# Kernel optimization log

Measured on AMD Instinct MI355X. Metric: run time of the kernel, lower is better.

## Reference

```python
import jax, jax.numpy as jnp
import numpy as np

B, N, NE = 16, 96, 256
ATOM, EDIM, HID, LAT, HEADS = 128, 16, 128, 128, 4
HD = LAT // HEADS
RBF, CUT, ZEMB, MAXZ = 16, 5.0, 32, 100
MUL0_IN, MUL1_IN = 64, 32      # irreps_node = 64x0e + 32x1o (dim 160)
MUL0_OUT, MUL1_OUT = 32, 16    # out irreps  = 32x0e + 16x1o (dim 80)
NODE_DIM = MUL0_IN + 3 * MUL1_IN
OUT_DIM = MUL0_OUT + 3 * MUL1_OUT
E_ATT = 1024
WNUM = MUL0_IN*MUL0_OUT + MUL0_IN*MUL1_OUT + MUL1_IN*MUL1_OUT + MUL1_IN*MUL0_OUT  # 4608


def _mlp3(x, w1, b1, w2, b2, w3, b3):
    x = jax.nn.silu(x @ w1 + b1)
    x = jax.nn.silu(x @ w2 + b2)
    return x @ w3 + b3


def setup_inputs() -> dict:
    key = jax.random.key(0)
    ks = jax.random.split(key, 40)
    s = 0.05  # scale params so deep MLP activations stay numerically sane
    d = {}
    d['h'] = jax.random.normal(ks[0], (B, N, ATOM), jnp.float32)
    d['h_full'] = jax.random.normal(ks[1], (B, N, NODE_DIM), jnp.float32)
    d['e_feat'] = jax.random.normal(ks[2], (NE, EDIM), jnp.float32)
    d['att_dist'] = jax.random.uniform(ks[3], (E_ATT,), jnp.float32)
    d['att_vec'] = jax.random.normal(ks[4], (E_ATT, 3), jnp.float32)
    d['z_emb_table'] = jax.random.normal(ks[5], (MAXZ + 1, ZEMB), jnp.float32) * s
    d['rw1'] = jax.random.normal(ks[6], (ZEMB + 1 + RBF, HID), jnp.float32) * s
    d['rb1'] = jnp.zeros((HID,), jnp.float32)
    d['rw2'] = jax.random.normal(ks[7], (HID, WNUM), jnp.float32) * s
    d['rb2'] = jnp.zeros((WNUM,), jnp.float32)
    d['ew1'] = jax.random.normal(ks[8], (EDIM, HID), jnp.float32) * s
    d['eb1'] = jnp.zeros((HID,), jnp.float32)
    d['ew2'] = jax.random.normal(ks[9], (HID, MUL0_OUT + MUL1_OUT), jnp.float32) * s
    d['eb2'] = jnp.zeros((MUL0_OUT + MUL1_OUT,), jnp.float32)
    d['qw1'] = jax.random.normal(ks[10], (ATOM + EDIM, HID), jnp.float32) * s
    d['qb1'] = jnp.zeros((HID,), jnp.float32)
    d['qw2'] = jax.random.normal(ks[11], (HID, HID), jnp.float32) * s
    d['qb2'] = jnp.zeros((HID,), jnp.float32)
    d['qw3'] = jax.random.normal(ks[12], (HID, LAT), jnp.float32) * s
    d['qb3'] = jnp.zeros((LAT,), jnp.float32)
    d['kw1'] = jax.random.normal(ks[13], (ATOM + ZEMB + 1 + RBF, HID), jnp.float32) * s
    d['kb1'] = jnp.zeros((HID,), jnp.float32)
    d['kw2'] = jax.random.normal(ks[14], (HID, HID), jnp.float32) * s
    d['kb2'] = jnp.zeros((HID,), jnp.float32)
    d['kw3'] = jax.random.normal(ks[15], (HID, LAT), jnp.float32) * s
    d['kb3'] = jnp.zeros((LAT,), jnp.float32)
    d['ow1'] = jax.random.normal(ks[16], (MUL0_OUT + MUL1_OUT, HID), jnp.float32) * s
    d['ob1'] = jnp.zeros((HID,), jnp.float32)
    d['ow2'] = jax.random.normal(ks[17], (HID, HID), jnp.float32) * s
    d['ob2'] = jnp.zeros((HID,), jnp.float32)
    d['ow3'] = jax.random.normal(ks[18], (HID, LAT), jnp.float32) * s
    d['ob3'] = jnp.zeros((LAT,), jnp.float32)
    d['z'] = jax.random.randint(ks[19], (B, N), 0, MAXZ)
    d['mask'] = jnp.ones((B, N), bool)
    d['absorber_index'] = jax.random.randint(ks[20], (B,), 0, N)
    d['att_dst'] = jnp.arange(E_ATT)  # unique flat indices into B*N
    return d


def reference(h, h_full, e_feat, att_dist, att_vec, z_emb_table,
              rw1, rb1, rw2, rb2, ew1, eb1, ew2, eb2,
              qw1, qb1, qw2, qb2, qw3, qb3,
              kw1, kb1, kw2, kb2, kw3, kb3,
              ow1, ob1, ow2, ob2, ow3, ob3,
              z, mask, absorber_index, att_dst):
    Bz, Na, Hd = h.shape
    F = Bz * Na
    nE = e_feat.shape[0]
    # scatter edge data into flat (B*N) atom slots
    am_flat = jnp.zeros((F,), bool).at[att_dst].set(True)
    d_flat = jnp.zeros((F,), h.dtype).at[att_dst].set(att_dist)
    v_flat = jnp.zeros((F, 3), h.dtype).at[att_dst].set(att_vec)
    att_mask = am_flat.reshape(Bz, Na) & mask
    # spherical harmonics (lmax=1, component normalization): Y0 = 1, Y1 = sqrt(3)*unit_vec
    un = v_flat / jnp.maximum(jnp.linalg.norm(v_flat, axis=-1, keepdims=True), 1e-8)
    y1 = jnp.sqrt(3.0) * un
    # Gaussian RBF on absorber->atom distance
    mu = jnp.linspace(0.0, CUT, RBF)
    delta = CUT / (RBF - 1)
    rbf = jnp.exp(-(d_flat[:, None] - mu) ** 2 / (2.0 * delta * delta))  # (F, RBF)
    zr = z_emb_table[z]                      # (B, N, ZEMB)
    zr_flat = zr.reshape(F, -1)
    is_abs = jnp.zeros((Bz, Na), h.dtype).at[jnp.arange(Bz), absorber_index].set(1.0)
    # radial MLP -> per-edge tensor-product weights
    w_in = jnp.concatenate([zr_flat, is_abs.reshape(F, 1), rbf], -1)
    tpw = jax.nn.silu(w_in @ rw1 + rb1) @ rw2 + rb2  # (F, WNUM)
    s1 = MUL0_IN * MUL0_OUT
    s2 = s1 + MUL0_IN * MUL1_OUT
    s3 = s2 + MUL1_IN * MUL1_OUT
    w00 = tpw[:, :s1].reshape(F, MUL0_IN, MUL0_OUT)   # 0e x 0e -> 0e
    w01 = tpw[:, s1:s2].reshape(F, MUL0_IN, MUL1_OUT) # 0e x 1o -> 1o
    w10 = tpw[:, s2:s3].reshape(F, MUL1_IN, MUL1_OUT) # 1o x 0e -> 1o
    w11 = tpw[:, s3:].reshape(F, MUL1_IN, MUL0_OUT)   # 1o x 1o -> 0e
    hf = h_full.reshape(F, -1)
    x0 = hf[:, :MUL0_IN]
    x1 = hf[:, MUL0_IN:].reshape(F, MUL1_IN, 3)
    alpha = 1.0 / jnp.sqrt(jnp.float32(MUL0_IN + MUL1_IN))  # path fan-in normalization
    c = 1.0 / jnp.sqrt(3.0)                                  # wigner-3j coeff for l=1 couplings
    out0 = alpha * (jnp.einsum('fi,fio->fo', x0, w00)
                    + c * jnp.einsum('fim,fm,fio->fo', x1, y1, w11))
    out1 = alpha * c * (jnp.einsum('fi,fm,fio->fom', x0, y1, w01)
                        + jnp.einsum('fim,fio->fom', x1, w10))
    v_irrep = jnp.concatenate([out0, out1.reshape(F, 3 * MUL1_OUT)], -1)  # (F, OUT_DIM)
    # cosine cutoff envelope + edge mask
    env = jnp.where(d_flat < CUT, 0.5 * (jnp.cos(jnp.pi * d_flat / CUT) + 1.0), 0.0)
    v_irrep = v_irrep * (am_flat.astype(h.dtype) * env)[:, None]
    # energy-conditioned per-irrep-channel modulation
    gates = jax.nn.silu(e_feat @ ew1 + eb1) @ ew2 + eb2  # (nE, 48)
    g_exp = jnp.concatenate([gates[:, :MUL0_OUT],
                             jnp.repeat(gates[:, MUL0_OUT:], 3, axis=-1)], -1)  # (nE, OUT_DIM)
    v_mod = (v_irrep[:, None, :] * g_exp[None]).reshape(Bz, Na, nE, OUT_DIM)
    # invariant multi-head scoring
    h_abs = h[jnp.arange(Bz), absorber_index]  # (B, H)
    q_in = jnp.concatenate([jnp.broadcast_to(h_abs[:, None], (Bz, nE, Hd)),
                            jnp.broadcast_to(e_feat[None], (Bz, nE, EDIM))], -1)
    q = _mlp3(q_in, qw1, qb1, qw2, qb2, qw3, qb3)  # (B, nE, LAT)
    atom_static = jnp.concatenate([h, zr, is_abs[..., None], rbf.reshape(Bz, Na, RBF)], -1)
    k = _mlp3(atom_static, kw1, kb1, kw2, kb2, kw3, kb3)  # (B, N, LAT)
    qh = q.reshape(Bz, nE, HEADS, HD)
    kh = k.reshape(Bz, Na, HEADS, HD)
    scores = (jnp.einsum('behd,bnhd->benh', qh, kh) * (HD ** -0.5)).mean(-1)  # (B, nE, N)
    m = att_mask[:, None, :]
    scores = jnp.where(m, scores, -1e9)
    attn = jax.nn.softmax(scores, axis=2) * m.astype(h.dtype)
    attn = attn / jnp.maximum(attn.sum(2, keepdims=True), 1e-8)
    out_irrep = jnp.einsum('ben,bnec->bec', attn, v_mod)  # (B, nE, OUT_DIM)
    # invariants: scalars + vector norms
    scal = out_irrep[..., :MUL0_OUT]
    vec = out_irrep[..., MUL0_OUT:].reshape(Bz, nE, MUL1_OUT, 3)
    inv = jnp.concatenate([scal, jnp.sqrt(jnp.sum(vec * vec, -1) + 1e-12)], -1)
    return _mlp3(inv, ow1, ob1, ow2, ob2, ow3, ob3)  # (B, nE, LAT)
```

## Files before the change

### kernel.cpp

```cpp
#include <hip/hip_runtime.h>
#include <hip/hip_fp16.h>
#include <math.h>

#define BB 16
#define NN 96
#define NE 256
#define FF (BB*NN)
#define ATOM 128
#define EDIM 16
#define HID 128
#define LAT 128
#define RBFN 16
#define CUTOFF 5.0f
#define ZEMB 32
#define E_ATT 1024
#define M0I 64
#define M1I 32
#define M0O 32
#define M1O 16
#define NODE_DIM 160
#define OUT_DIM 80
#define INVD 48
#define WNUM 4608
#define SEG1 2048
#define SEG2 3072
#define SEG3 3584

#define NODE_BLKS (FF/4)
#define EC_BLKS 16
#define HABS_BLKS 2
#define GATE_BLKS 16
#define STAGE1_BLKS (NODE_BLKS + EC_BLKS + HABS_BLKS + GATE_BLKS)

#define TPW_BLKS (36*32)
#define GQ_BLKS (TPW_BLKS + 512)

__device__ __forceinline__ float silu_f(float x) { return x / (1.0f + expf(-x)); }

__global__ __launch_bounds__(1024) void k_prep(
    const int* __restrict__ att_dst, const float* __restrict__ att_dist,
    const float* __restrict__ att_vec,
    int* __restrict__ inv, float* __restrict__ y1E, float* __restrict__ envE)
{
    int t = threadIdx.x;
    inv[t] = -1;
    if (t < FF - 1024) inv[1024 + t] = -1;
    {
        float d = att_dist[t];
        envE[t] = (d < CUTOFF) ? 0.5f*(cosf(3.14159265358979323846f*d/CUTOFF) + 1.0f) : 0.0f;
        float vx = att_vec[3*t], vy = att_vec[3*t+1], vz = att_vec[3*t+2];
        float nrm = sqrtf(vx*vx + vy*vy + vz*vz);
        float is = 1.0f / fmaxf(nrm, 1e-8f);
        const float s3 = 1.7320508075688772f;
        y1E[3*t]   = s3*vx*is;
        y1E[3*t+1] = s3*vy*is;
        y1E[3*t+2] = s3*vz*is;
    }
    __syncthreads();
    inv[att_dst[t]] = t;
}

__global__ __launch_bounds__(256) void k_stage1(
    const float* __restrict__ h, const float* __restrict__ z_emb, const int* __restrict__ z,
    const int* __restrict__ absorber, const float* __restrict__ e_feat,
    const int* __restrict__ inv, const float* __restrict__ att_dist,
    const float* __restrict__ rw1, const float* __restrict__ rb1,
    const float* __restrict__ kw1, const float* __restrict__ kb1,
    const float* __restrict__ kw2, const float* __restrict__ kb2,
    const float* __restrict__ kw3, const float* __restrict__ kb3,
    const float* __restrict__ qw1,
    const float* __restrict__ ew1, const float* __restrict__ eb1,
    const float* __restrict__ ew2, const float* __restrict__ eb2,
    float* __restrict__ hiddenE, float* __restrict__ kmatw,
    float* __restrict__ ecw, float* __restrict__ habs1w, float* __restrict__ gexp)
{
    __shared__ float smem[3488];
    int blk = blockIdx.x;
    int t = threadIdx.x;

    if (blk < NODE_BLKS) {
        float (*sin1)[184] = (float(*)[184])smem;
        float (*l1S)[128]  = (float(*)[128])(smem + 736);
        float (*l2S)[128]  = (float(*)[128])(smem + 736 + 512);
        int f0 = blk * 4;
        {
            int n = t >> 6, i2 = t & 63;
            float2 hv = *(const float2*)&h[(f0 + n)*ATOM + i2*2];
            sin1[n][i2*2] = hv.x; sin1[n][i2*2 + 1] = hv.y;
        }
        if (t < 128) {
            int n = t >> 5, j = t & 31;
            sin1[n][ATOM + j] = z_emb[z[f0 + n]*ZEMB + j];
        }
        if (t < 64) {
            int n = t >> 4, j = t & 15;
            int e = inv[f0 + n];
            float d = ((unsigned)e < E_ATT) ? att_dist[e] : 0.0f;
            const float delta = CUTOFF / (RBFN - 1);
            float diff = d - j*delta;
            sin1[n][ATOM + ZEMB + 1 + j] = expf(-diff*diff / (2.0f*delta*delta));
        }
        if (t < 4) {
            int f = f0 + t;
            int b = f / NN, nn = f - b*NN;
            sin1[t][ATOM + ZEMB] = (absorber[b] == nn) ? 1.0f : 0.0f;
        }
        __syncthreads();
        int n = t >> 6;
        int c2 = (t & 63) * 2;
        int e = inv[f0 + n];
        bool att_ = ((unsigned)e < E_ATT);
        if (att_) {
            float2 a0 = *(const float2*)&rb1[c2];
            float2 a1 = make_float2(0.f, 0.f);
            #pragma unroll 8
            for (int i = 0; i < 48; i += 2) {
                float x0v = sin1[n][ATOM + i], x1v = sin1[n][ATOM + i + 1];
                float2 w0 = *(const float2*)&rw1[i*HID + c2];
                float2 w1 = *(const float2*)&rw1[(i+1)*HID + c2];
                a0.x += x0v*w0.x; a0.y += x0v*w0.y;
                a1.x += x1v*w1.x; a1.y += x1v*w1.y;
            }
            {
                float x0v = sin1[n][ATOM + 48];
                float2 w0 = *(const float2*)&rw1[48*HID + c2];
                a0.x += x0v*w0.x; a0.y += x0v*w0.y;
            }
            float2 o; o.x = silu_f(a0.x + a1.x); o.y = silu_f(a0.y + a1.y);
            *(float2*)&hiddenE[e*HID + c2] = o;
        }
        {
            float2 a0 = *(const float2*)&kb1[c2];
            float2 a1 = make_float2(0.f, 0.f);
            #pragma unroll 8
            for (int i = 0; i < 176; i += 2) {
                float x0v = sin1[n][i], x1v = sin1[n][i + 1];
                float2 w0 = *(const float2*)&kw1[i*HID + c2];
                float2 w1 = *(const float2*)&kw1[(i+1)*HID + c2];
                a0.x += x0v*w0.x; a0.y += x0v*w0.y;
                a1.x += x1v*w1.x; a1.y += x1v*w1.y;
            }
            {
                float x0v = sin1[n][176];
                float2 w0 = *(const float2*)&kw1[176*HID + c2];
                a0.x += x0v*w0.x; a0.y += x0v*w0.y;
            }
            l1S[n][c2] = silu_f(a0.x + a1.x); l1S[n][c2+1] = silu_f(a0.y + a1.y);
        }
        __syncthreads();
        {
            float2 a0 = *(const float2*)&kb2[c2];
            float2 a1 = make_float2(0.f, 0.f);
            #pragma unroll 8
            for (int i = 0; i < HID; i += 2) {
                float x0v = l1S[n][i], x1v = l1S[n][i + 1];
                float2 w0 = *(const float2*)&kw2[i*HID + c2];
                float2 w1 = *(const float2*)&kw2[(i+1)*HID + c2];
                a0.x += x0v*w0.x; a0.y += x0v*w0.y;
                a1.x += x1v*w1.x; a1.y += x1v*w1.y;
            }
            l2S[n][c2] = silu_f(a0.x + a1.x); l2S[n][c2+1] = silu_f(a0.y + a1.y);
        }
        __syncthreads();
        {
            float2 a0 = *(const float2*)&kb3[c2];
            float2 a1 = make_float2(0.f, 0.f);
            #pragma unroll 8
            for (int i = 0; i < HID; i += 2) {
                float x0v = l2S[n][i], x1v = l2S[n][i + 1];
                float2 w0 = *(const float2*)&kw3[i*HID + c2];
                float2 w1 = *(const float2*)&kw3[(i+1)*HID + c2];
                a0.x += x0v*w0.x; a0.y += x0v*w0.y;
                a1.x += x1v*w1.x; a1.y += x1v*w1.y;
            }
            float2 o; o.x = a0.x + a1.x; o.y = a0.y + a1.y;
            *(float2*)&kmatw[(f0 + n)*HID + c2] = o;
        }
    } else if (blk < NODE_BLKS + EC_BLKS) {
        float (*ef)[16] = (float(*)[16])smem;
        int e0 = (blk - NODE_BLKS) * 16;
        { int e = t >> 4, i = t & 15; ef[e][i] = e_feat[(e0 + e)*EDIM + i]; }
        __syncthreads();
        int r = t >> 4, c0 = (t & 15)*8;
        float4 a0 = make_float4(0,0,0,0), a1 = a0;
        #pragma unroll
        for (int i = 0; i < EDIM; i++) {
            float a = ef[r][i];
            float4 w0 = *(const float4*)&qw1[(ATOM + i)*HID + c0];
            float4 w1 = *(const float4*)&qw1[(ATOM + i)*HID + c0 + 4];
            a0.x += a*w0.x; a0.y += a*w0.y; a0.z += a*w0.z; a0.w += a*w0.w;
            a1.x += a*w1.x; a1.y += a*w1.y; a1.z += a*w1.z; a1.w += a*w1.w;
        }
        *(float4*)&ecw[(e0 + r)*HID + c0] = a0;
        *(float4*)&ecw[(e0 + r)*HID + c0 + 4] = a1;
    } else if (blk < NODE_BLKS + EC_BLKS + HABS_BLKS) {
        float (*hr)[128] = (float(*)[128])smem;
        int b0 = (blk - NODE_BLKS - EC_BLKS) * 8;
        {
            int r = t >> 5, i4 = t & 31;
            int b = b0 + r;
            int a = absorber[b];
            *(float4*)&hr[r][i4*4] = *(const float4*)&h[(b*NN + a)*ATOM + i4*4];
        }
        __syncthreads();
        int r = t >> 5, c0 = (t & 31)*4;
        float4 a0 = make_float4(0,0,0,0), a1 = a0;
        #pragma unroll 8
        for (int i = 0; i < ATOM; i += 2) {
            float x0v = hr[r][i], x1v = hr[r][i+1];
            float4 w0 = *(const float4*)&qw1[i*HID + c0];
            float4 w1 = *(const float4*)&qw1[(i+1)*HID + c0];
            a0.x += x0v*w0.x; a0.y += x0v*w0.y; a0.z += x0v*w0.z; a0.w += x0v*w0.w;
            a1.x += x1v*w1.x; a1.y += x1v*w1.y; a1.z += x1v*w1.z; a1.w += x1v*w1.w;
        }
        float4 o;
        o.x = a0.x + a1.x; o.y = a0.y + a1.y; o.z = a0.z + a1.z; o.w = a0.w + a1.w;
        *(float4*)&habs1w[(b0 + r)*HID + c0] = o;
    } else {
        float (*ef)[16]   = (float(*)[16])smem;
        float (*l1g)[128] = (float(*)[128])(smem + 256);
        float (*gg)[48]   = (float(*)[48])(smem + 256 + 2048);
        int e0 = (blk - NODE_BLKS - EC_BLKS - HABS_BLKS) * 16;
        { int e = t >> 4, i = t & 15; ef[e][i] = e_feat[(e0 + e)*EDIM + i]; }
        __syncthreads();
        int r = t >> 4, c0 = (t & 15)*8;
        {
            float4 a0 = *(const float4*)&eb1[c0];
            float4 a1 = *(const float4*)&eb1[c0 + 4];
            #pragma unroll
            for (int i = 0; i < EDIM; i++) {
                float a = ef[r][i];
                float4 w0 = *(const float4*)&ew1[i*HID + c0];
                float4 w1 = *(const float4*)&ew1[i*HID + c0 + 4];
                a0.x += a*w0.x; a0.y += a*w0.y; a0.z += a*w0.z; a0.w += a*w0.w;
                a1.x += a*w1.x; a1.y += a*w1.y; a1.z += a*w1.z; a1.w += a*w1.w;
            }
            l1g[r][c0]   = silu_f(a0.x); l1g[r][c0+1] = silu_f(a0.y);
            l1g[r][c0+2] = silu_f(a0.z); l1g[r][c0+3] = silu_f(a0.w);
            l1g[r][c0+4] = silu_f(a1.x); l1g[r][c0+5] = silu_f(a1.y);
            l1g[r][c0+6] = silu_f(a1.z); l1g[r][c0+7] = silu_f(a1.w);
        }
        __syncthreads();
        for (int u = t; u < 16*48; u += 256) {
            int e = u / 48, j = u - 48*(u/48);
            float acc = eb2[j];
            #pragma unroll 4
            for (int i = 0; i < HID; i++) acc += l1g[e][i]*ew2[i*48 + j];
            gg[e][j] = acc;
        }
        __syncthreads();
        for (int u = t; u < 16*80; u += 256) {
            int e = u / 80, cc = u - 80*(u/80);
            gexp[(e0 + e)*OUT_DIM + cc] = (cc < M0O) ? gg[e][cc] : gg[e][M0O + (cc - M0O)/3];
        }
    }
}

__global__ __launch_bounds__(256) void k_gq(
    const float* __restrict__ hiddenE, const float* __restrict__ rw2, const float* __restrict__ rb2,
    const float* __restrict__ habs1, const float* __restrict__ ec, const float* __restrict__ qb1,
    const float* __restrict__ qw2, const float* __restrict__ qb2,
    const float* __restrict__ qw3, const float* __restrict__ qb3,
    __half* __restrict__ tpwE, float* __restrict__ qmat)
{
    __shared__ float smem[5248];
    int blk = blockIdx.x;
    int t = threadIdx.x;
    if (blk < TPW_BLKS) {
        float* As = smem;
        float* Bs = smem + 1152;
        int col0 = (blk % 36) * 128;
        int row0 = (blk / 36) * 32;
        float4 acc[4];
        for (int j = 0; j < 4; j++) acc[j] = make_float4(0,0,0,0);
        int tc = t & 31, tr = t >> 5;
        for (int k0 = 0; k0 < HID; k0 += 32) {
            {
                int rr = t >> 3, k4 = t & 7;
                float4 hv = *(const float4*)&hiddenE[(row0 + rr)*HID + k0 + k4*4];
                As[rr*36 + k4*4]   = hv.x; As[rr*36 + k4*4+1] = hv.y;
                As[rr*36 + k4*4+2] = hv.z; As[rr*36 + k4*4+3] = hv.w;
            }
            for (int p = 0; p < 4; p++) {
                int idx = t + 256*p;
                int kk = idx >> 5, c4 = idx & 31;
                *(float4*)&Bs[kk*128 + c4*4] = *(const float4*)&rw2[(k0 + kk)*WNUM + col0 + c4*4];
            }
            __syncthreads();
            for (int kk = 0; kk < 32; kk++) {
                float4 bv = *(float4*)&Bs[kk*128 + tc*4];
                #pragma unroll
                for (int j = 0; j < 4; j++) {
                    float a = As[(tr*4 + j)*36 + kk];
                    acc[j].x += a*bv.x; acc[j].y += a*bv.y; acc[j].z += a*bv.z; acc[j].w += a*bv.w;
                }
            }
            __syncthreads();
        }
        float4 bias = *(const float4*)&rb2[col0 + tc*4];
        for (int j = 0; j < 4; j++) {
            int r = row0 + tr*4 + j;
            __half2* d2 = (__half2*)&tpwE[(long)r*WNUM + col0 + tc*4];
            d2[0] = __floats2half2_rn(acc[j].x + bias.x, acc[j].y + bias.y);
            d2[1] = __floats2half2_rn(acc[j].z + bias.z, acc[j].w + bias.w);
        }
    } else {
        float* l1S = smem;
        float* l2S = smem + 1024;
        int r0 = (blk - TPW_BLKS) * 8;
        for (int p = 0; p < 4; p++) {
            int idx = t + 256*p;
            int rr = idx >> 7, i = idx & 127;
            int be = r0 + rr; int b = be >> 8; int e = be & 255;
            l1S[rr*128 + i] = silu_f(habs1[b*HID + i] + ec[e*HID + i] + qb1[i]);
        }
        __syncthreads();
        int r = t >> 5, c0 = (t & 31)*4;
        {
            float4 a0 = *(const float4*)&qb2[c0];
            float4 a1 = make_float4(0,0,0,0);
            #pragma unroll 8
            for (int i = 0; i < HID; i += 2) {
                float x0v = l1S[r*128 + i], x1v = l1S[r*128 + i+1];
                float4 w0 = *(const float4*)&qw2[i*HID + c0];
                float4 w1 = *(const float4*)&qw2[(i+1)*HID + c0];
                a0.x += x0v*w0.x; a0.y += x0v*w0.y; a0.z += x0v*w0.z; a0.w += x0v*w0.w;
                a1.x += x1v*w1.x; a1.y += x1v*w1.y; a1.z += x1v*w1.z; a1.w += x1v*w1.w;
            }
            l2S[r*128 + c0]   = silu_f(a0.x + a1.x); l2S[r*128 + c0+1] = silu_f(a0.y + a1.y);
            l2S[r*128 + c0+2] = silu_f(a0.z + a1.z); l2S[r*128 + c0+3] = silu_f(a0.w + a1.w);
        }
        __syncthreads();
        {
            float4 a0 = *(const float4*)&qb3[c0];
            float4 a1 = make_float4(0,0,0,0);
            #pragma unroll 8
            for (int i = 0; i < HID; i += 2) {
                float x0v = l2S[r*128 + i], x1v = l2S[r*128 + i+1];
                float4 w0 = *(const float4*)&qw3[i*HID + c0];
                float4 w1 = *(const float4*)&qw3[(i+1)*HID + c0];
                a0.x += x0v*w0.x; a0.y += x0v*w0.y; a0.z += x0v*w0.z; a0.w += x0v*w0.w;
                a1.x += x1v*w1.x; a1.y += x1v*w1.y; a1.z += x1v*w1.z; a1.w += x1v*w1.w;
            }
            float4 o;
            o.x = a0.x + a1.x; o.y = a0.y + a1.y; o.z = a0.z + a1.z; o.w = a0.w + a1.w;
            *(float4*)&qmat[(r0 + r)*LAT + c0] = o;
        }
    }
}

__global__ __launch_bounds__(256) void k_score(
    const float* __restrict__ qmat, const float* __restrict__ kmat, const int* __restrict__ inv,
    float* __restrict__ scoresW)
{
    int b  = blockIdx.x >> 3;
    int e0 = (blockIdx.x & 7) * 32;
    int t = threadIdx.x;
    __shared__ float Qs[32][132];
    __shared__ float Ks[96][132];
    __shared__ float mS[NN];

    for (int p = 0; p < 4; p++) {
        int idx = t + 256*p; int e = idx >> 5, i4 = idx & 31;
        *(float4*)&Qs[e][i4*4] = *(const float4*)&qmat[(b*NE + e0 + e)*LAT + i4*4];
    }
    for (int p = 0; p < 12; p++) {
        int idx = t + 256*p; int n = idx >> 5, i4 = idx & 31;
        *(float4*)&Ks[n][i4*4] = *(const float4*)&kmat[(b*NN + n)*LAT + i4*4];
    }
    if (t < NN) mS[t] = ((unsigned)inv[b*NN + t] < E_ATT) ? 1.0f : 0.0f;
    __syncthreads();

    int te = t >> 5;
    int tn = t & 31;
    float acc[4][3] = {};
    for (int i = 0; i < LAT; i++) {
        float bv0 = Ks[tn][i], bv1 = Ks[tn + 32][i], bv2 = Ks[tn + 64][i];
        #pragma unroll
        for (int j = 0; j < 4; j++) {
            float a = Qs[te*4 + j][i];
            acc[j][0] += a*bv0; acc[j][1] += a*bv1; acc[j][2] += a*bv2;
        }
    }
    const float scale = 0.04419417382415922f;
    #pragma unroll
    for (int j = 0; j < 4; j++)
        #pragma unroll
        for (int jj = 0; jj < 3; jj++) {
            int n = tn + 32*jj;
            float s = (mS[n] != 0.f) ? acc[j][jj]*scale : -1e9f;
            scoresW[((b*NE) + e0 + te*4 + j)*NN + n] = s;
        }
}

__global__ __launch_bounds__(256) void k_attf(
    const float* __restrict__ scoresW, const int* __restrict__ inv,
    const float* __restrict__ virr, const float* __restrict__ gexp,
    const float* __restrict__ ow1, const float* __restrict__ ob1,
    const float* __restrict__ ow2, const float* __restrict__ ob2,
    const float* __restrict__ ow3, const float* __restrict__ ob3,
    float* __restrict__ out)
{
    int b  = blockIdx.x >> 5;
    int e0 = (blockIdx.x & 31) * 8;
    int t = threadIdx.x;
    __shared__ float aS[8][100];
    __shared__ float gS[8][84];
    __shared__ float ocS[8][84];
    __shared__ float mS[NN];
    __shared__ float inS[8][INVD];
    __shared__ float l1S[8][HID];
    __shared__ float l2S[8][HID];

    for (int p = 0; p < 3; p++) {
        int idx = t + 256*p;
        int el = idx / NN, n = idx - NN*(idx/NN);
        aS[el][n] = scoresW[((b*NE) + e0 + el)*NN + n];
    }
    if (t < 160) {
        int el = t / 20, c4 = t - 20*(t/20);
        *(float4*)&gS[el][c4*4] = *(const float4*)&gexp[(e0 + el)*OUT_DIM + c4*4];
    }
    if (t < NN) mS[t] = ((unsigned)inv[b*NN + t] < E_ATT) ? 1.0f : 0.0f;
    __syncthreads();

    {
        int el = t >> 5;
        int ng = t & 31;
        float s0 = aS[el][ng], s1 = aS[el][ng + 32], s2 = aS[el][ng + 64];
        float m0 = mS[ng], m1 = mS[ng + 32], m2 = mS[ng + 64];
        float mx = fmaxf(s0, fmaxf(s1, s2));
        #pragma unroll
        for (int off = 1; off < 32; off <<= 1) mx = fmaxf(mx, __shfl_xor(mx, off));
        float e0v = expf(s0 - mx), e1v = expf(s1 - mx), e2v = expf(s2 - mx);
        float sm = e0v + e1v + e2v;
        #pragma unroll
        for (int off = 1; off < 32; off <<= 1) sm += __shfl_xor(sm, off);
        float r = 1.0f / sm;
        float p0 = m0*e0v*r, p1 = m1*e1v*r, p2 = m2*e2v*r;
        float ss = p0 + p1 + p2;
        #pragma unroll
        for (int off = 1; off < 32; off <<= 1) ss += __shfl_xor(ss, off);
        float is = 1.0f / fmaxf(ss, 1e-8f);
        aS[el][ng]      = p0*is;
        aS[el][ng + 32] = p1*is;
        aS[el][ng + 64] = p2*is;
    }
    __syncthreads();

    if (t < 160) {
        int el = t / 20, c4 = t - 20*(t/20);
        const float* vp = virr + (long)b*NN*OUT_DIM + c4*4;
        float4 acc = make_float4(0,0,0,0);
        #pragma unroll 4
        for (int n = 0; n < NN; n++) {
            float a = aS[el][n];
            float4 v = *(const float4*)&vp[n*OUT_DIM];
            acc.x += a*v.x; acc.y += a*v.y; acc.z += a*v.z; acc.w += a*v.w;
        }
        float4 g = *(float4*)&gS[el][c4*4];
        float4 o; o.x = acc.x*g.x; o.y = acc.y*g.y; o.z = acc.z*g.z; o.w = acc.w*g.w;
        *(float4*)&ocS[el][c4*4] = o;
    }
    __syncthreads();

    for (int u = t; u < 8*INVD; u += 256) {
        int el = u / INVD, j = u - INVD*(u/INVD);
        float val;
        if (j < M0O) val = ocS[el][j];
        else {
            int o = j - M0O;
            float x = ocS[el][M0O + 3*o], y = ocS[el][M0O + 3*o + 1], zz = ocS[el][M0O + 3*o + 2];
            val = sqrtf(x*x + y*y + zz*zz + 1e-12f);
        }
        inS[el][j] = val;
    }
    __syncthreads();

    int r = t >> 5, c0 = (t & 31)*4;
    {
        float4 a0 = *(const float4*)&ob1[c0];
        float4 a1 = make_float4(0,0,0,0);
        #pragma unroll 8
        for (int i = 0; i < INVD; i += 2) {
            float x0v = inS[r][i], x1v = inS[r][i+1];
            float4 w0 = *(const float4*)&ow1[i*HID + c0];
            float4 w1 = *(const float4*)&ow1[(i+1)*HID + c0];
            a0.x += x0v*w0.x; a0.y += x0v*w0.y; a0.z += x0v*w0.z; a0.w += x0v*w0.w;
            a1.x += x1v*w1.x; a1.y += x1v*w1.y; a1.z += x1v*w1.z; a1.w += x1v*w1.w;
        }
        l1S[r][c0]   = silu_f(a0.x + a1.x); l1S[r][c0+1] = silu_f(a0.y + a1.y);
        l1S[r][c0+2] = silu_f(a0.z + a1.z); l1S[r][c0+3] = silu_f(a0.w + a1.w);
    }
    __syncthreads();
    {
        float4 a0 = *(const float4*)&ob2[c0];
        float4 a1 = make_float4(0,0,0,0);
        #pragma unroll 8
        for (int i = 0; i < HID; i += 2) {
            float x0v = l1S[r][i], x1v = l1S[r][i+1];
            float4 w0 = *(const float4*)&ow2[i*HID + c0];
            float4 w1 = *(const float4*)&ow2[(i+1)*HID + c0];
            a0.x += x0v*w0.x; a0.y += x0v*w0.y; a0.z += x0v*w0.z; a0.w += x0v*w0.w;
            a1.x += x1v*w1.x; a1.y += x1v*w1.y; a1.z += x1v*w1.z; a1.w += x1v*w1.w;
        }
        l2S[r][c0]   = silu_f(a0.x + a1.x); l2S[r][c0+1] = silu_f(a0.y + a1.y);
        l2S[r][c0+2] = silu_f(a0.z + a1.z); l2S[r][c0+3] = silu_f(a0.w + a1.w);
    }
    __syncthreads();
    {
        float4 a0 = *(const float4*)&ob3[c0];
        float4 a1 = make_float4(0,0,0,0);
        #pragma unroll 8
        for (int i = 0; i < HID; i += 2) {
            float x0v = l2S[r][i], x1v = l2S[r][i+1];
            float4 w0 = *(const float4*)&ow3[i*HID + c0];
            float4 w1 = *(const float4*)&ow3[(i+1)*HID + c0];
            a0.x += x0v*w0.x; a0.y += x0v*w0.y; a0.z += x0v*w0.z; a0.w += x0v*w0.w;
            a1.x += x1v*w1.x; a1.y += x1v*w1.y; a1.z += x1v*w1.z; a1.w += x1v*w1.w;
        }
        float4 o;
        o.x = a0.x + a1.x; o.y = a0.y + a1.y; o.z = a0.z + a1.z; o.w = a0.w + a1.w;
        *(float4*)&out[((b*NE + e0) + r)*LAT + c0] = o;
    }
}

__global__ __launch_bounds__(128) void k_tp(
    const float* __restrict__ h_full, const __half* __restrict__ tpwE,
    const int* __restrict__ att_dst,
    const float* __restrict__ envE, const float* __restrict__ y1E,
    float* __restrict__ virr)
{
    int e = blockIdx.x; int t = threadIdx.x;
    int f = att_dst[e];
    __shared__ float x0[M0I];
    __shared__ float x1f[M1I*3];
    __shared__ float xy[M1I];
    __shared__ float y1s[3];
    const float* hf = h_full + f*NODE_DIM;
    if (t < M0I) x0[t] = hf[t];
    if (t < M1I*3) x1f[t] = hf[M0I + t];
    if (t < 3) y1s[t] = y1E[3*e + t];
    __syncthreads();
    if (t < M1I) xy[t] = x1f[3*t]*y1s[0] + x1f[3*t+1]*y1s[1] + x1f[3*t+2]*y1s[2];
    __syncthreads();
    float scale = envE[e];
    const __half* w = tpwE + (long)e*WNUM;
    const float alpha = 0.10206207261596575f;
    const float cc = 0.5773502691896258f;
    if (t < M0O) {
        float t00 = 0.f, t11 = 0.f;
        #pragma unroll 4
        for (int i = 0; i < M0I; i++) t00 += x0[i]*__half2float(w[i*M0O + t]);
        #pragma unroll 4
        for (int i = 0; i < M1I; i++) t11 += xy[i]*__half2float(w[SEG3 + i*M0O + t]);
        virr[f*OUT_DIM + t] = alpha*(t00 + cc*t11)*scale;
    } else if (t < M0O + 3*M1O) {
        int idx = t - M0O; int o = idx/3, m = idx - 3*o;
        float t01 = 0.f, t10 = 0.f;
        #pragma unroll 4
        for (int i = 0; i < M0I; i++) t01 += x0[i]*__half2float(w[SEG1 + i*M1O + o]);
        #pragma unroll 4
        for (int i = 0; i < M1I; i++) t10 += x1f[i*3 + m]*__half2float(w[SEG2 + i*M1O + o]);
        virr[f*OUT_DIM + t] = alpha*cc*(t01*y1s[m] + t10)*scale;
    }
}

extern "C" void kernel_launch(void* const* d_in, const int* in_sizes, int n_in,
                              void* d_out, int out_size, void* d_ws, size_t ws_size,
                              hipStream_t stream) {
    const float* h        = (const float*)d_in[0];
    const float* h_full   = (const float*)d_in[1];
    const float* e_feat   = (const float*)d_in[2];
    const float* att_dist = (const float*)d_in[3];
    const float* att_vec  = (const float*)d_in[4];
    const float* z_emb    = (const float*)d_in[5];
    const float* rw1 = (const float*)d_in[6];  const float* rb1 = (const float*)d_in[7];
    const float* rw2 = (const float*)d_in[8];  const float* rb2 = (const float*)d_in[9];
    const float* ew1 = (const float*)d_in[10]; const float* eb1 = (const float*)d_in[11];
    const float* ew2 = (const float*)d_in[12]; const float* eb2 = (const float*)d_in[13];
    const float* qw1 = (const float*)d_in[14]; const float* qb1 = (const float*)d_in[15];
    const float* qw2 = (const float*)d_in[16]; const float* qb2 = (const float*)d_in[17];
    const float* qw3 = (const float*)d_in[18]; const float* qb3 = (const float*)d_in[19];
    const float* kw1 = (const float*)d_in[20]; const float* kb1 = (const float*)d_in[21];
    const float* kw2 = (const float*)d_in[22]; const float* kb2 = (const float*)d_in[23];
    const float* kw3 = (const float*)d_in[24]; const float* kb3 = (const float*)d_in[25];
    const float* ow1 = (const float*)d_in[26]; const float* ob1 = (const float*)d_in[27];
    const float* ow2 = (const float*)d_in[28]; const float* ob2 = (const float*)d_in[29];
    const float* ow3 = (const float*)d_in[30]; const float* ob3 = (const float*)d_in[31];
    const int* z        = (const int*)d_in[32];
    const int* absorber = (const int*)d_in[34];
    const int* att_dst  = (const int*)d_in[35];

    float* ws = (float*)d_ws;
    int*   inv     = (int*)ws;
    float* y1E     = ws + 1536;
    float* envE    = ws + 4608;
    float* hiddenE = ws + 5632;
    float* kmat    = ws + 136704;
    float* qmat    = ws + 333312;
    float* gexp    = ws + 857600;
    float* virr    = ws + 878080;
    float* habs1   = ws + 1000960;
    float* ec      = ws + 1003008;
    float* scoresW = ws + 1035776;
    __half* tpwE   = (__half*)(ws + 1428992);

    float* out = (float*)d_out;

    k_prep<<<1, 1024, 0, stream>>>(att_dst, att_dist, att_vec, inv, y1E, envE);
    k_stage1<<<STAGE1_BLKS, 256, 0, stream>>>(h, z_emb, z, absorber, e_feat, inv, att_dist,
                                              rw1, rb1, kw1, kb1, kw2, kb2, kw3, kb3,
                                              qw1, ew1, eb1, ew2, eb2,
                                              hiddenE, kmat, ec, habs1, gexp);
    k_gq<<<GQ_BLKS, 256, 0, stream>>>(hiddenE, rw2, rb2, habs1, ec, qb1,
                                      qw2, qb2, qw3, qb3, tpwE, qmat);
    k_score<<<128, 256, 0, stream>>>(qmat, kmat, inv, scoresW);
    k_tp<<<E_ATT, 128, 0, stream>>>(h_full, tpwE, att_dst, envE, y1E, virr);
    k_attf<<<BB*32, 256, 0, stream>>>(scoresW, inv, virr, gexp,
                                      ow1, ob1, ow2, ob2, ow3, ob3, out);
}
```

Measured before the change: 251.7 us.

## Compute radial tensor-product weight GEMM with fp16 MFMA instead of FP32 FMA

Replaces the FP32 shared-memory tiled GEMM (1024x128 @ 128x4608) with a matrix-core version built on mfma_f32_16x16x32_f16. Each wave loads its operands straight from global memory. The hidden activations are now written as fp16. A new prep stage transposes rw2 into a K-major fp16 copy on every call, and the single-block prep work is spread over 256-thread blocks. The aim is to cut the FP32 FMA cost of the dominant GEMM. In exchange, inputs are rounded to fp16 and each call pays for an extra transpose pass and uncoalesced half-precision output stores.

```diff
diff --git a/kernel.cpp b/kernel.cpp
--- a/kernel.cpp
+++ b/kernel.cpp
@@ -32,32 +32,55 @@
 #define GATE_BLKS 16
 #define STAGE1_BLKS (NODE_BLKS + EC_BLKS + HABS_BLKS + GATE_BLKS)
 
-#define TPW_BLKS (36*32)
-#define GQ_BLKS (TPW_BLKS + 512)
+#define MFMA_BLKS (36*16)
+#define MQ_BLKS (MFMA_BLKS + 512)
+
+typedef _Float16 half8_t __attribute__((ext_vector_type(8)));
+typedef float float4v __attribute__((ext_vector_type(4)));
 
 __device__ __forceinline__ float silu_f(float x) { return x / (1.0f + expf(-x)); }
 
-__global__ __launch_bounds__(1024) void k_prep(
+__global__ __launch_bounds__(256) void k_prep(
+    const float* __restrict__ rw2,
     const int* __restrict__ att_dst, const float* __restrict__ att_dist,
     const float* __restrict__ att_vec,
-    int* __restrict__ inv, float* __restrict__ y1E, float* __restrict__ envE)
+    __half* __restrict__ rw2T, int* __restrict__ inv,
+    float* __restrict__ y1E, float* __restrict__ envE)
 {
+    int blk = blockIdx.x;
     int t = threadIdx.x;
-    inv[t] = -1;
-    if (t < FF - 1024) inv[1024 + t] = -1;
-    {
-        float d = att_dist[t];
-        envE[t] = (d < CUTOFF) ? 0.5f*(cosf(3.14159265358979323846f*d/CUTOFF) + 1.0f) : 0.0f;
-        float vx = att_vec[3*t], vy = att_vec[3*t+1], vz = att_vec[3*t+2];
+    if (blk < 144) {
+        __shared__ __half lds[64][66];
+        int nt = blk % 72, kt = blk / 72;
+        int n0 = nt*64, k0 = kt*64;
+        for (int p = 0; p < 16; p++) {
+            int idx = t + 256*p;
+            int kk = idx >> 6, nn = idx & 63;
+            lds[nn][kk] = __float2half(rw2[(k0+kk)*WNUM + n0+nn]);
+        }
+        __syncthreads();
+        for (int p = 0; p < 16; p++) {
+            int idx = t + 256*p;
+            int nn = idx >> 6, kk = idx & 63;
+            rw2T[(n0+nn)*HID + k0+kk] = lds[nn][kk];
+        }
+        return;
+    }
+    for (int p = 0; p < 6; p++) inv[t + 256*p] = -1;
+    for (int p = 0; p < 4; p++) {
+        int e = t + 256*p;
+        float d = att_dist[e];
+        envE[e] = (d < CUTOFF) ? 0.5f*(cosf(3.14159265358979323846f*d/CUTOFF) + 1.0f) : 0.0f;
+        float vx = att_vec[3*e], vy = att_vec[3*e+1], vz = att_vec[3*e+2];
         float nrm = sqrtf(vx*vx + vy*vy + vz*vz);
         float is = 1.0f / fmaxf(nrm, 1e-8f);
         const float s3 = 1.7320508075688772f;
-        y1E[3*t]   = s3*vx*is;
-        y1E[3*t+1] = s3*vy*is;
-        y1E[3*t+2] = s3*vz*is;
-    }
-    __syncthreads();
-    inv[att_dst[t]] = t;
+        y1E[3*e]   = s3*vx*is;
+        y1E[3*e+1] = s3*vy*is;
+        y1E[3*e+2] = s3*vz*is;
+    }
+    __syncthreads();
+    for (int p = 0; p < 4; p++) { int e = t + 256*p; inv[att_dst[e]] = e; }
 }
 
 __global__ __launch_bounds__(256) void k_stage1(
@@ -71,7 +94,7 @@
     const float* __restrict__ qw1,
     const float* __restrict__ ew1, const float* __restrict__ eb1,
     const float* __restrict__ ew2, const float* __restrict__ eb2,
-    float* __restrict__ hiddenE, float* __restrict__ kmatw,
+    __half* __restrict__ hiddenH, float* __restrict__ kmatw,
     float* __restrict__ ecw, float* __restrict__ habs1w, float* __restrict__ gexp)
 {
     __shared__ float smem[3488];
@@ -126,8 +149,8 @@
                 float2 w0 = *(const float2*)&rw1[48*HID + c2];
                 a0.x += x0v*w0.x; a0.y += x0v*w0.y;
             }
-            float2 o; o.x = silu_f(a0.x + a1.x); o.y = silu_f(a0.y + a1.y);
-            *(float2*)&hiddenE[e*HID + c2] = o;
+            *(__half2*)&hiddenH[e*HID + c2] =
+                __floats2half2_rn(silu_f(a0.x + a1.x), silu_f(a0.y + a1.y));
         }
         {
             float2 a0 = *(const float2*)&kb1[c2];
@@ -256,58 +279,49 @@
     }
 }
 
-__global__ __launch_bounds__(256) void k_gq(
-    const float* __restrict__ hiddenE, const float* __restrict__ rw2, const float* __restrict__ rb2,
+__global__ __launch_bounds__(256) void k_mq(
+    const __half* __restrict__ hiddenH, const __half* __restrict__ rw2T,
+    const float* __restrict__ rb2,
     const float* __restrict__ habs1, const float* __restrict__ ec, const float* __restrict__ qb1,
     const float* __restrict__ qw2, const float* __restrict__ qb2,
     const float* __restrict__ qw3, const float* __restrict__ qb3,
     __half* __restrict__ tpwE, float* __restrict__ qmat)
 {
-    __shared__ float smem[5248];
+    __shared__ float smem[2048];
     int blk = blockIdx.x;
     int t = threadIdx.x;
-    if (blk < TPW_BLKS) {
-        float* As = smem;
-        float* Bs = smem + 1152;
-        int col0 = (blk % 36) * 128;
-        int row0 = (blk / 36) * 32;
-        float4 acc[4];
-        for (int j = 0; j < 4; j++) acc[j] = make_float4(0,0,0,0);
-        int tc = t & 31, tr = t >> 5;
-        for (int k0 = 0; k0 < HID; k0 += 32) {
-            {
-                int rr = t >> 3, k4 = t & 7;
-                float4 hv = *(const float4*)&hiddenE[(row0 + rr)*HID + k0 + k4*4];
-                As[rr*36 + k4*4]   = hv.x; As[rr*36 + k4*4+1] = hv.y;
-                As[rr*36 + k4*4+2] = hv.z; As[rr*36 + k4*4+3] = hv.w;
-            }
-            for (int p = 0; p < 4; p++) {
-                int idx = t + 256*p;
-                int kk = idx >> 5, c4 = idx & 31;
-                *(float4*)&Bs[kk*128 + c4*4] = *(const float4*)&rw2[(k0 + kk)*WNUM + col0 + c4*4];
-            }
-            __syncthreads();
-            for (int kk = 0; kk < 32; kk++) {
-                float4 bv = *(float4*)&Bs[kk*128 + tc*4];
-                #pragma unroll
-                for (int j = 0; j < 4; j++) {
-                    float a = As[(tr*4 + j)*36 + kk];
-                    acc[j].x += a*bv.x; acc[j].y += a*bv.y; acc[j].z += a*bv.z; acc[j].w += a*bv.w;
-                }
-            }
-            __syncthreads();
-        }
-        float4 bias = *(const float4*)&rb2[col0 + tc*4];
-        for (int j = 0; j < 4; j++) {
-            int r = row0 + tr*4 + j;
-            __half2* d2 = (__half2*)&tpwE[(long)r*WNUM + col0 + tc*4];
-            d2[0] = __floats2half2_rn(acc[j].x + bias.x, acc[j].y + bias.y);
-            d2[1] = __floats2half2_rn(acc[j].z + bias.z, acc[j].w + bias.w);
+    if (blk < MFMA_BLKS) {
+        int colTile = blk % 36;
+        int rowGrp  = blk / 36;
+        int wv = t >> 6;
+        int lane = t & 63;
+        int m0 = (rowGrp*4 + wv) * 16;
+        int n0 = colTile * 128;
+        int mrow = lane & 15, quad = lane >> 4;
+        const _Float16* hp = (const _Float16*)hiddenH + (m0 + mrow)*HID + quad*8;
+        half8_t af[4];
+        #pragma unroll
+        for (int kc = 0; kc < 4; kc++) af[kc] = *(const half8_t*)(hp + kc*32);
+        #pragma unroll
+        for (int nt = 0; nt < 8; nt++) {
+            const _Float16* bp = (const _Float16*)rw2T + (n0 + nt*16 + mrow)*HID + quad*8;
+            float4v acc = {0.f, 0.f, 0.f, 0.f};
+            #pragma unroll
+            for (int kc = 0; kc < 4; kc++) {
+                half8_t bf = *(const half8_t*)(bp + kc*32);
+                acc = __builtin_amdgcn_mfma_f32_16x16x32_f16(af[kc], bf, acc, 0, 0, 0);
+            }
+            int col = n0 + nt*16 + mrow;
+            float bias = rb2[col];
+            int rbase = m0 + quad*4;
+            #pragma unroll
+            for (int r = 0; r < 4; r++)
+                tpwE[(long)(rbase + r)*WNUM + col] = __float2half(acc[r] + bias);
         }
     } else {
         float* l1S = smem;
         float* l2S = smem + 1024;
-        int r0 = (blk - TPW_BLKS) * 8;
+        int r0 = (blk - MFMA_BLKS) * 8;
         for (int p = 0; p < 4; p++) {
             int idx = t + 256*p;
             int rr = idx >> 7, i = idx & 127;
@@ -596,24 +610,25 @@
     int*   inv     = (int*)ws;
     float* y1E     = ws + 1536;
     float* envE    = ws + 4608;
-    float* hiddenE = ws + 5632;
-    float* kmat    = ws + 136704;
-    float* qmat    = ws + 333312;
-    float* gexp    = ws + 857600;
-    float* virr    = ws + 878080;
-    float* habs1   = ws + 1000960;
-    float* ec      = ws + 1003008;
-    float* scoresW = ws + 1035776;
-    __half* tpwE   = (__half*)(ws + 1428992);
+    float* kmat    = ws + 5632;
+    float* qmat    = ws + 202240;
+    float* gexp    = ws + 726528;
+    float* virr    = ws + 747008;
+    float* habs1   = ws + 869888;
+    float* ec      = ws + 871936;
+    float* scoresW = ws + 904704;
+    __half* tpwE   = (__half*)(ws + 1297920);
+    __half* rw2T   = (__half*)(ws + 3657216);
+    __half* hiddenH= (__half*)(ws + 3952128);
 
     float* out = (float*)d_out;
 
-    k_prep<<<1, 1024, 0, stream>>>(att_dst, att_dist, att_vec, inv, y1E, envE);
+    k_prep<<<145, 256, 0, stream>>>(rw2, att_dst, att_dist, att_vec, rw2T, inv, y1E, envE);
     k_stage1<<<STAGE1_BLKS, 256, 0, stream>>>(h, z_emb, z, absorber, e_feat, inv, att_dist,
                                               rw1, rb1, kw1, kb1, kw2, kb2, kw3, kb3,
                                               qw1, ew1, eb1, ew2, eb2,
-                                              hiddenE, kmat, ec, habs1, gexp);
-    k_gq<<<GQ_BLKS, 256, 0, stream>>>(hiddenE, rw2, rb2, habs1, ec, qb1,
+                                              hiddenH, kmat, ec, habs1, gexp);
+    k_mq<<<MQ_BLKS, 256, 0, stream>>>(hiddenH, rw2T, rb2, habs1, ec, qb1,
                                       qw2, qb2, qw3, qb3, tpwE, qmat);
     k_score<<<128, 256, 0, stream>>>(qmat, kmat, inv, scoresW);
     k_tp<<<E_ATT, 128, 0, stream>>>(h_full, tpwE, att_dst, envE, y1E, virr);
```

Result: no change. 250.5 us (-0.5%).
